# Kernel tuning notes

Measured on AMD Instinct MI355X. Metric: run time of the kernel, lower is better.

## Reference

```python
import jax, jax.numpy as jnp
import numpy as np

B, C_IN, T = 64, 9, 4096
HIDDEN, OUT = 128, 10
NEW_T = T // 4            # two MaxPool1d(2) stages
N_NODES = B * NEW_T       # 65536 flattened nodes
N_EDGES = 524288


def setup_inputs() -> dict:
    key = jax.random.key(0)
    ks = jax.random.split(key, 8)
    def w(k, sh, fan):
        return jax.random.normal(k, sh, jnp.float32) * (1.0 / np.sqrt(fan))
    return {
        "x": jax.random.normal(ks[0], (B, C_IN, T), jnp.float32),
        "edge_index": jax.random.randint(ks[1], (2, N_EDGES), 0, N_NODES, dtype=jnp.int32),
        "conv1_w": w(ks[2], (16, C_IN, 5), C_IN * 5),
        "conv1_b": jnp.zeros((16,), jnp.float32),
        "conv2_w": w(ks[3], (32, 16, 5), 16 * 5),
        "conv2_b": jnp.zeros((32,), jnp.float32),
        "gcn1_w": w(ks[4], (32, HIDDEN), 32),
        "gcn1_b": jnp.zeros((HIDDEN,), jnp.float32),
        "gcn2_w": w(ks[5], (HIDDEN, HIDDEN), HIDDEN),
        "gcn2_b": jnp.zeros((HIDDEN,), jnp.float32),
        "cls_w": w(ks[6], (HIDDEN, OUT), HIDDEN),
        "cls_b": jnp.zeros((OUT,), jnp.float32),
    }


def _conv1d(x, w, b):
    # x: [B, C, T], w: [O, I, K], 'same' padding (pad=2, k=5)
    y = jax.lax.conv_general_dilated(x, w, (1,), [(2, 2)],
                                     dimension_numbers=("NCH", "OIH", "NCH"))
    return y + b[None, :, None]


def _maxpool2(x):
    return jax.lax.reduce_window(x, -jnp.inf, jax.lax.max, (1, 1, 2), (1, 1, 2), "VALID")


def _gcn(x, w, b, src, dst):
    # PyG GCNConv: add self-loops, symmetric D^{-1/2}(A+I)D^{-1/2} X W + b
    h = x @ w
    deg = jnp.zeros((N_NODES,), x.dtype).at[dst].add(1.0) + 1.0  # +1 for self-loop
    dinv = jax.lax.rsqrt(deg)
    coef = dinv[src] * dinv[dst]                      # [E]
    agg = jnp.zeros_like(h).at[dst].add(h[src] * coef[:, None])
    agg = agg + h * (dinv * dinv)[:, None]            # self-loop contribution
    return agg + b


def reference(x, edge_index, conv1_w, conv1_b, conv2_w, conv2_b,
              gcn1_w, gcn1_b, gcn2_w, gcn2_b, cls_w, cls_b):
    h = _maxpool2(jax.nn.relu(_conv1d(x, conv1_w, conv1_b)))   # [B,16,T/2]
    h = _maxpool2(jax.nn.relu(_conv1d(h, conv2_w, conv2_b)))   # [B,32,T/4]
    feats = h.transpose(0, 2, 1).reshape(-1, 32)               # [B*NEW_T, 32]
    src, dst = edge_index[0], edge_index[1]
    g = jax.nn.relu(_gcn(feats, gcn1_w, gcn1_b, src, dst))
    g = jax.nn.relu(_gcn(g, gcn2_w, gcn2_b, src, dst))
    pooled = g.reshape(B, NEW_T, HIDDEN).mean(axis=1)          # mean over nodes per graph
    return pooled @ cls_w + cls_b                              # [B, OUT]
```

## Files before the change

### kernel.cpp

```cpp
#include <hip/hip_runtime.h>
#include <hip/hip_bf16.h>

typedef __hip_bfloat16 bf16;
typedef unsigned short ushort8_v __attribute__((ext_vector_type(8)));
typedef short bf16x8 __attribute__((ext_vector_type(8)));
typedef float f32x4 __attribute__((ext_vector_type(4)));

#define N_B     64
#define C_IN    9
#define T0      4096
#define C1      16
#define T1      2048
#define C2      32
#define T2      1024
#define N_NODES 65536
#define N_EDGES 524288
#define HID     128
#define OUT_C   10
#define SLOT_CAP 32

__device__ __forceinline__ float us2f(unsigned short u) {
  union { unsigned int i; float f; } c; c.i = ((unsigned int)u) << 16; return c.f;
}
__device__ __forceinline__ unsigned short f2us(float f) {
  bf16 h = __float2bfloat16(f);
  unsigned short u;
  __builtin_memcpy(&u, &h, 2);
  return u;
}


__global__ __launch_bounds__(256) void init_kernel(int* __restrict__ cnt, float* __restrict__ pooled,
                                                   const float* __restrict__ W1, const float* __restrict__ W2,
                                                   unsigned short* __restrict__ W1T, unsigned short* __restrict__ W2T)
{
  int gid = blockIdx.x * 256 + threadIdx.x;
  if (gid < N_NODES) cnt[gid] = 0;
  if (gid < N_B * HID) pooled[gid] = 0.f;
  if (gid < HID * HID) {
    int j = gid >> 7, k = gid & 127;
    W2T[j * HID + k] = f2us(W2[(size_t)k * HID + j]);
  }
  if (gid >= 32768 && gid < 32768 + HID * 32) {
    int i = gid - 32768;
    int j = i >> 5, k = i & 31;
    W1T[j * 32 + k] = f2us(W1[(size_t)k * HID + j]);
  }
}

__global__ __launch_bounds__(256) void conv1_scatter_kernel(const float* __restrict__ x, const float* __restrict__ w1,
                                                            const float* __restrict__ b1,
                                                            const int* __restrict__ ei, int* __restrict__ cnt,
                                                            unsigned short* __restrict__ slots,
                                                            unsigned short* __restrict__ y1)
{
  __shared__ float sx[C_IN * 136];
  __shared__ float sw[45 * 17];
  __shared__ float sb[C1];
  int tid = threadIdx.x;
  if (blockIdx.x < 2048) {
    int e = blockIdx.x * 256 + tid;
    int d = ei[N_EDGES + e];
    int s = ei[e];
    int r = atomicAdd(&cnt[d], 1);
    if (r < SLOT_CAP) slots[((size_t)d << 5) + r] = (unsigned short)s;
    return;
  }
  int blk = blockIdx.x - 2048;
  int b = blk >> 5;
  int P0 = (blk & 31) << 6;
  int t0 = 2 * P0 - 2;
  for (int i = tid; i < C_IN * 132; i += 256) {
    int c = i / 132, j = i % 132;
    int t = t0 + j;
    sx[c * 136 + j] = (t >= 0 && t < T0) ? x[(size_t)(b * C_IN + c) * T0 + t] : 0.f;
  }
  for (int i = tid; i < C1 * 45; i += 256) sw[(i % 45) * 17 + i / 45] = w1[i];
  if (tid < C1) sb[tid] = b1[tid];
  __syncthreads();

  int o = tid & 15, pg = tid >> 4;
  float bias = sb[o];
  float a[8];
  #pragma unroll
  for (int i = 0; i < 8; ++i) a[i] = bias;
  #pragma unroll
  for (int c = 0; c < C_IN; ++c) {
    float xv[12];
    #pragma unroll
    for (int q = 0; q < 3; ++q)
      *(float4*)&xv[4 * q] = *(const float4*)&sx[c * 136 + 8 * pg + 4 * q];
    const float* wr = &sw[(c * 5) * 17 + o];
    float w0 = wr[0], w1_ = wr[17], w2_ = wr[34], w3_ = wr[51], w4_ = wr[68];
    #pragma unroll
    for (int m = 0; m < 8; ++m)
      a[m] += xv[m]*w0 + xv[m+1]*w1_ + xv[m+2]*w2_ + xv[m+3]*w3_ + xv[m+4]*w4_;
  }
  ushort4 r;
  r.x = f2us(fmaxf(fmaxf(a[0], a[1]), 0.f));
  r.y = f2us(fmaxf(fmaxf(a[2], a[3]), 0.f));
  r.z = f2us(fmaxf(fmaxf(a[4], a[5]), 0.f));
  r.w = f2us(fmaxf(fmaxf(a[6], a[7]), 0.f));
  *(ushort4*)&y1[(size_t)(b * C1 + o) * T1 + P0 + 4 * pg] = r;
}

__global__ __launch_bounds__(256) void conv2_kernel(const unsigned short* __restrict__ y1, const float* __restrict__ w2,
                                                    const float* __restrict__ b2, const int* __restrict__ cnt,
                                                    unsigned short* __restrict__ feats)
{
  __shared__ float sy[C1 * 72];
  __shared__ float sw[80 * 33];
  __shared__ float sb[C2];
  int tid = threadIdx.x;
  int b = blockIdx.x >> 5;
  int Q0 = (blockIdx.x & 31) << 5;
  int t0 = 2 * Q0 - 2;
  for (int i = tid; i < C1 * 68; i += 256) {
    int c = i / 68, j = i % 68;
    int t = t0 + j;
    sy[c * 72 + j] = (t >= 0 && t < T1) ? us2f(y1[(size_t)(b * C1 + c) * T1 + t]) : 0.f;
  }
  for (int i = tid; i < C2 * 80; i += 256) sw[(i % 80) * 33 + i / 80] = w2[i];
  if (tid < C2) sb[tid] = b2[tid];
  __syncthreads();

  int o = tid & 31, pg = tid >> 5;
  float bias = sb[o];
  float a[8];
  #pragma unroll
  for (int i = 0; i < 8; ++i) a[i] = bias;
  #pragma unroll
  for (int c = 0; c < C1; ++c) {
    float yv[12];
    #pragma unroll
    for (int q = 0; q < 3; ++q)
      *(float4*)&yv[4 * q] = *(const float4*)&sy[c * 72 + 8 * pg + 4 * q];
    const float* wr = &sw[(c * 5) * 33 + o];
    float w0 = wr[0], w1_ = wr[33], w2_ = wr[66], w3_ = wr[99], w4_ = wr[132];
    #pragma unroll
    for (int m = 0; m < 8; ++m)
      a[m] += yv[m]*w0 + yv[m+1]*w1_ + yv[m+2]*w2_ + yv[m+3]*w3_ + yv[m+4]*w4_;
  }
  #pragma unroll
  for (int i = 0; i < 4; ++i) {
    int node = (b << 10) + Q0 + 4 * pg + i;
    float dv = rsqrtf((float)cnt[node] + 1.0f);
    feats[(size_t)node * C2 + o] = f2us(fmaxf(fmaxf(a[2*i], a[2*i+1]), 0.f) * dv);
  }
}

__global__ __launch_bounds__(256) void aggX_kernel(const unsigned short* __restrict__ F, const int* __restrict__ cnt,
                                                   const unsigned short* __restrict__ slots,
                                                   unsigned short* __restrict__ aggXb)
{
  int tid = threadIdx.x;
  int node = (blockIdx.x << 6) + (tid >> 2);
  int jq = (tid & 3) << 3;
  int cn = cnt[node];
  float dn = rsqrtf((float)cn + 1.0f);
  float acc[8];
  {
    ushort8_v r = *(const ushort8_v*)(F + (size_t)node * C2 + jq);
    #pragma unroll
    for (int k = 0; k < 8; ++k) acc[k] = us2f(r[k]);
  }
  const unsigned short* sl = slots + ((size_t)node << 5);
  int e1 = min(cn, SLOT_CAP);
  int e = 0;
  for (; e + 2 <= e1; e += 2) {
    int s0 = sl[e], s1 = sl[e + 1];
    ushort8_v r0 = *(const ushort8_v*)(F + (size_t)s0 * C2 + jq);
    ushort8_v r1 = *(const ushort8_v*)(F + (size_t)s1 * C2 + jq);
    #pragma unroll
    for (int k = 0; k < 8; ++k) acc[k] += us2f(r0[k]) + us2f(r1[k]);
  }
  if (e < e1) {
    int s0 = sl[e];
    ushort8_v r0 = *(const ushort8_v*)(F + (size_t)s0 * C2 + jq);
    #pragma unroll
    for (int k = 0; k < 8; ++k) acc[k] += us2f(r0[k]);
  }
  ushort8_v o;
  #pragma unroll
  for (int k = 0; k < 8; ++k) o[k] = f2us(acc[k] * dn);
  *(ushort8_v*)(aggXb + (size_t)node * C2 + jq) = o;
}

__global__ __launch_bounds__(256) void gemm12_kernel(const unsigned short* __restrict__ aggXb,
                                                     const unsigned short* __restrict__ W1T,
                                                     const float* __restrict__ gb1,
                                                     const unsigned short* __restrict__ W2T,
                                                     const int* __restrict__ cnt,
                                                     unsigned short* __restrict__ Hb)
{
  __shared__ unsigned short sG[64 * 132];
  int tid = threadIdx.x;
  int w = tid >> 6, l = tid & 63;
  int lr = l & 15, lk = l >> 4;
  int n0b = blockIdx.x << 6;

  {
    int nb = w << 4;
    bf16x8 af = *(const bf16x8*)((const short*)aggXb + (size_t)(n0b + nb + lr) * C2 + lk * 8);
    #pragma unroll
    for (int jt = 0; jt < 8; ++jt) {
      bf16x8 bfr = *(const bf16x8*)((const short*)W1T + (jt * 16 + lr) * 32 + lk * 8);
      f32x4 acc = {0.f, 0.f, 0.f, 0.f};
      acc = __builtin_amdgcn_mfma_f32_16x16x32_bf16(af, bfr, acc, 0, 0, 0);
      float bj = gb1[jt * 16 + lr];
      #pragma unroll
      for (int r = 0; r < 4; ++r)
        sG[(nb + lk * 4 + r) * 132 + jt * 16 + lr] = f2us(fmaxf(acc[r] + bj, 0.f));
    }
  }
  __syncthreads();

  {
    int jb = w << 5;
    bf16x8 bfr[2][4];
    #pragma unroll
    for (int jtt = 0; jtt < 2; ++jtt)
      #pragma unroll
      for (int ks = 0; ks < 4; ++ks)
        bfr[jtt][ks] = *(const bf16x8*)((const short*)W2T + (size_t)(jb + jtt * 16 + lr) * HID + ks * 32 + lk * 8);
    #pragma unroll
    for (int nt = 0; nt < 4; ++nt) {
      bf16x8 afr[4];
      #pragma unroll
      for (int ks = 0; ks < 4; ++ks)
        afr[ks] = *(const bf16x8*)((const short*)sG + (nt * 16 + lr) * 132 + ks * 32 + lk * 8);
      int rowb = n0b + nt * 16 + lk * 4;
      int4 c4 = *(const int4*)&cnt[rowb];
      float dvr[4] = { rsqrtf((float)c4.x + 1.f), rsqrtf((float)c4.y + 1.f),
                       rsqrtf((float)c4.z + 1.f), rsqrtf((float)c4.w + 1.f) };
      #pragma unroll
      for (int jtt = 0; jtt < 2; ++jtt) {
        f32x4 acc = {0.f, 0.f, 0.f, 0.f};
        #pragma unroll
        for (int ks = 0; ks < 4; ++ks)
          acc = __builtin_amdgcn_mfma_f32_16x16x32_bf16(afr[ks], bfr[jtt][ks], acc, 0, 0, 0);
        #pragma unroll
        for (int r = 0; r < 4; ++r)
          Hb[(size_t)(rowb + r) * HID + jb + jtt * 16 + lr] = f2us(acc[r] * dvr[r]);
      }
    }
  }
}

__global__ __launch_bounds__(256) void agg2_pool_kernel(const unsigned short* __restrict__ Hb, const int* __restrict__ cnt,
                                                        const unsigned short* __restrict__ slots,
                                                        const float* __restrict__ bias, float* __restrict__ pooled)
{
  __shared__ float red[16][HID];
  int tid = threadIdx.x;
  int g = tid >> 4;
  int jq = (tid & 15) << 3;
  int node = (blockIdx.x << 4) + g;
  int cn = cnt[node];
  float dn = rsqrtf((float)cn + 1.0f);
  float acc[8];
  {
    ushort8_v r = *(const ushort8_v*)(Hb + (size_t)node * HID + jq);
    #pragma unroll
    for (int k = 0; k < 8; ++k) acc[k] = us2f(r[k]);
  }
  const unsigned short* sl = slots + ((size_t)node << 5);
  int e1 = min(cn, SLOT_CAP);
  int e = 0;
  for (; e + 2 <= e1; e += 2) {
    int s0 = sl[e], s1 = sl[e + 1];
    ushort8_v r0 = *(const ushort8_v*)(Hb + (size_t)s0 * HID + jq);
    ushort8_v r1 = *(const ushort8_v*)(Hb + (size_t)s1 * HID + jq);
    #pragma unroll
    for (int k = 0; k < 8; ++k) acc[k] += us2f(r0[k]) + us2f(r1[k]);
  }
  if (e < e1) {
    int s0 = sl[e];
    ushort8_v r0 = *(const ushort8_v*)(Hb + (size_t)s0 * HID + jq);
    #pragma unroll
    for (int k = 0; k < 8; ++k) acc[k] += us2f(r0[k]);
  }
  #pragma unroll
  for (int k = 0; k < 8; ++k)
    red[g][jq + k] = fmaxf(dn * acc[k] + bias[jq + k], 0.f);
  __syncthreads();
  if (tid < HID) {
    float s = 0.f;
    #pragma unroll
    for (int g2 = 0; g2 < 16; ++g2) s += red[g2][tid];
    int b = blockIdx.x >> 6;
    atomicAdd(&pooled[b * HID + tid], s * (1.0f / 1024.0f));
  }
}


__global__ __launch_bounds__(64) void cls_kernel(const float* __restrict__ pooled, const float* __restrict__ w,
                                                 const float* __restrict__ cb, float* __restrict__ out)
{
  int b = blockIdx.x, o = threadIdx.x;
  if (o < OUT_C) {
    float acc = cb[o];
    for (int i = 0; i < HID; ++i)
      acc += pooled[b * HID + i] * w[i * OUT_C + o];
    out[b * OUT_C + o] = acc;
  }
}


extern "C" void kernel_launch(void* const* d_in, const int* in_sizes, int n_in,
                              void* d_out, int out_size, void* d_ws, size_t ws_size,
                              hipStream_t stream)
{
  const float* x    = (const float*)d_in[0];
  const int*   ei   = (const int*)d_in[1];
  const float* c1w  = (const float*)d_in[2];
  const float* c1b  = (const float*)d_in[3];
  const float* c2w  = (const float*)d_in[4];
  const float* c2b  = (const float*)d_in[5];
  const float* g1w  = (const float*)d_in[6];
  const float* g1b  = (const float*)d_in[7];
  const float* g2w  = (const float*)d_in[8];
  const float* g2b  = (const float*)d_in[9];
  const float* clsw = (const float*)d_in[10];
  const float* clsb = (const float*)d_in[11];
  float* outp = (float*)d_out;

  char* ws = (char*)d_ws;
  size_t off_b = 0;
  auto alloc = [&](size_t bytes) { void* p = ws + off_b; off_b = (off_b + bytes + 255) & ~(size_t)255; return p; };
  int*   cnt    = (int*)  alloc((size_t)N_NODES * 4);
  unsigned short* slots = (unsigned short*)alloc((size_t)N_NODES * SLOT_CAP * 2);
  unsigned short* w1t   = (unsigned short*)alloc((size_t)HID * 32 * 2);
  unsigned short* w2t   = (unsigned short*)alloc((size_t)HID * HID * 2);
  unsigned short* y1    = (unsigned short*)alloc((size_t)N_B * C1 * T1 * 2);
  unsigned short* feats = (unsigned short*)alloc((size_t)N_NODES * C2 * 2);
  unsigned short* aggXb = (unsigned short*)alloc((size_t)N_NODES * C2 * 2);
  unsigned short* H     = (unsigned short*)alloc((size_t)N_NODES * HID * 2);
  float* pooled = (float*)alloc((size_t)N_B * HID * 4);
  (void)ws_size; (void)in_sizes; (void)n_in; (void)out_size;

  init_kernel         <<<256, 256, 0, stream>>>(cnt, pooled, g1w, g2w, w1t, w2t);
  conv1_scatter_kernel<<<4096, 256, 0, stream>>>(x, c1w, c1b, ei, cnt, slots, y1);

  conv2_kernel<<<2048, 256, 0, stream>>>(y1, c2w, c2b, cnt, feats);

  aggX_kernel<<<N_NODES / 64, 256, 0, stream>>>(feats, cnt, slots, aggXb);

  gemm12_kernel<<<N_NODES / 64, 256, 0, stream>>>(aggXb, w1t, g1b, w2t, cnt, H);

  agg2_pool_kernel<<<N_NODES / 16, 256, 0, stream>>>(H, cnt, slots, g2b, pooled);

  cls_kernel<<<N_B, 64, 0, stream>>>(pooled, clsw, clsb, outp);
}
```

Baseline: 110.8 us.

## Fuse first GCN aggregation into GEMM kernel and fold init work elsewhere

The separate first-layer aggregation kernel is removed. Each gemm12 lane now gathers its node's neighbor features for its 8-wide K slice and builds the MFMA A fragment directly, so the aggX intermediate never goes through global memory. The weight transposes move into extra blocks of the conv1/scatter launch, and the counter and pooled zeroing become hipMemsetAsync calls. Both gather loops are unrolled to four loads in flight. This saves a launch and an intermediate round trip, but adds two memset operations, and the gather in gemm12 may be less parallel than the old standalone kernel.

After: 107.3 us. 1.03x faster.

```diff
diff --git a/kernel.cpp b/kernel.cpp
--- a/kernel.cpp
+++ b/kernel.cpp
@@ -29,30 +29,14 @@
   return u;
 }
 
-
-__global__ __launch_bounds__(256) void init_kernel(int* __restrict__ cnt, float* __restrict__ pooled,
-                                                   const float* __restrict__ W1, const float* __restrict__ W2,
-                                                   unsigned short* __restrict__ W1T, unsigned short* __restrict__ W2T)
-{
-  int gid = blockIdx.x * 256 + threadIdx.x;
-  if (gid < N_NODES) cnt[gid] = 0;
-  if (gid < N_B * HID) pooled[gid] = 0.f;
-  if (gid < HID * HID) {
-    int j = gid >> 7, k = gid & 127;
-    W2T[j * HID + k] = f2us(W2[(size_t)k * HID + j]);
-  }
-  if (gid >= 32768 && gid < 32768 + HID * 32) {
-    int i = gid - 32768;
-    int j = i >> 5, k = i & 31;
-    W1T[j * 32 + k] = f2us(W1[(size_t)k * HID + j]);
-  }
-}
-
 __global__ __launch_bounds__(256) void conv1_scatter_kernel(const float* __restrict__ x, const float* __restrict__ w1,
                                                             const float* __restrict__ b1,
                                                             const int* __restrict__ ei, int* __restrict__ cnt,
                                                             unsigned short* __restrict__ slots,
-                                                            unsigned short* __restrict__ y1)
+                                                            unsigned short* __restrict__ y1,
+                                                            const float* __restrict__ W1, const float* __restrict__ W2,
+                                                            unsigned short* __restrict__ W1T,
+                                                            unsigned short* __restrict__ W2T)
 {
   __shared__ float sx[C_IN * 136];
   __shared__ float sw[45 * 17];
@@ -66,6 +50,26 @@
     if (r < SLOT_CAP) slots[((size_t)d << 5) + r] = (unsigned short)s;
     return;
   }
+  if (blockIdx.x >= 4096) {
+    int blk = blockIdx.x - 4096;
+    if (blk < 16) {
+      int base = blk * 1024 + tid * 4;
+      #pragma unroll
+      for (int i = 0; i < 4; ++i) {
+        int idx = base + i;
+        int j = idx >> 7, k = idx & 127;
+        W2T[j * HID + k] = f2us(W2[(size_t)k * HID + j]);
+      }
+    } else {
+      #pragma unroll
+      for (int i = 0; i < 16; ++i) {
+        int idx = tid * 16 + i;
+        int j = idx >> 5, k = idx & 31;
+        W1T[j * 32 + k] = f2us(W1[(size_t)k * HID + j]);
+      }
+    }
+    return;
+  }
   int blk = blockIdx.x - 2048;
   int b = blk >> 5;
   int P0 = (blk & 31) << 6;
@@ -149,48 +153,12 @@
   }
 }
 
-__global__ __launch_bounds__(256) void aggX_kernel(const unsigned short* __restrict__ F, const int* __restrict__ cnt,
-                                                   const unsigned short* __restrict__ slots,
-                                                   unsigned short* __restrict__ aggXb)
-{
-  int tid = threadIdx.x;
-  int node = (blockIdx.x << 6) + (tid >> 2);
-  int jq = (tid & 3) << 3;
-  int cn = cnt[node];
-  float dn = rsqrtf((float)cn + 1.0f);
-  float acc[8];
-  {
-    ushort8_v r = *(const ushort8_v*)(F + (size_t)node * C2 + jq);
-    #pragma unroll
-    for (int k = 0; k < 8; ++k) acc[k] = us2f(r[k]);
-  }
-  const unsigned short* sl = slots + ((size_t)node << 5);
-  int e1 = min(cn, SLOT_CAP);
-  int e = 0;
-  for (; e + 2 <= e1; e += 2) {
-    int s0 = sl[e], s1 = sl[e + 1];
-    ushort8_v r0 = *(const ushort8_v*)(F + (size_t)s0 * C2 + jq);
-    ushort8_v r1 = *(const ushort8_v*)(F + (size_t)s1 * C2 + jq);
-    #pragma unroll
-    for (int k = 0; k < 8; ++k) acc[k] += us2f(r0[k]) + us2f(r1[k]);
-  }
-  if (e < e1) {
-    int s0 = sl[e];
-    ushort8_v r0 = *(const ushort8_v*)(F + (size_t)s0 * C2 + jq);
-    #pragma unroll
-    for (int k = 0; k < 8; ++k) acc[k] += us2f(r0[k]);
-  }
-  ushort8_v o;
-  #pragma unroll
-  for (int k = 0; k < 8; ++k) o[k] = f2us(acc[k] * dn);
-  *(ushort8_v*)(aggXb + (size_t)node * C2 + jq) = o;
-}
-
-__global__ __launch_bounds__(256) void gemm12_kernel(const unsigned short* __restrict__ aggXb,
+__global__ __launch_bounds__(256) void gemm12_kernel(const unsigned short* __restrict__ F,
+                                                     const int* __restrict__ cnt,
+                                                     const unsigned short* __restrict__ slots,
                                                      const unsigned short* __restrict__ W1T,
                                                      const float* __restrict__ gb1,
                                                      const unsigned short* __restrict__ W2T,
-                                                     const int* __restrict__ cnt,
                                                      unsigned short* __restrict__ Hb)
 {
   __shared__ unsigned short sG[64 * 132];
@@ -201,7 +169,39 @@
 
   {
     int nb = w << 4;
-    bf16x8 af = *(const bf16x8*)((const short*)aggXb + (size_t)(n0b + nb + lr) * C2 + lk * 8);
+    int node = n0b + nb + lr;
+    int cn = cnt[node];
+    float dn = rsqrtf((float)cn + 1.0f);
+    int koff = lk << 3;
+    float accf[8];
+    {
+      ushort8_v r = *(const ushort8_v*)(F + (size_t)node * C2 + koff);
+      #pragma unroll
+      for (int k = 0; k < 8; ++k) accf[k] = us2f(r[k]);
+    }
+    const unsigned short* sl = slots + ((size_t)node << 5);
+    int e1 = min(cn, SLOT_CAP);
+    int e = 0;
+    for (; e + 4 <= e1; e += 4) {
+      int s0 = sl[e], s1 = sl[e + 1], s2 = sl[e + 2], s3 = sl[e + 3];
+      ushort8_v r0 = *(const ushort8_v*)(F + (size_t)s0 * C2 + koff);
+      ushort8_v r1 = *(const ushort8_v*)(F + (size_t)s1 * C2 + koff);
+      ushort8_v r2 = *(const ushort8_v*)(F + (size_t)s2 * C2 + koff);
+      ushort8_v r3 = *(const ushort8_v*)(F + (size_t)s3 * C2 + koff);
+      #pragma unroll
+      for (int k = 0; k < 8; ++k)
+        accf[k] += (us2f(r0[k]) + us2f(r1[k])) + (us2f(r2[k]) + us2f(r3[k]));
+    }
+    for (; e < e1; ++e) {
+      int s0 = sl[e];
+      ushort8_v r0 = *(const ushort8_v*)(F + (size_t)s0 * C2 + koff);
+      #pragma unroll
+      for (int k = 0; k < 8; ++k) accf[k] += us2f(r0[k]);
+    }
+    bf16x8 af;
+    #pragma unroll
+    for (int k = 0; k < 8; ++k) af[k] = (short)f2us(accf[k] * dn);
+
     #pragma unroll
     for (int jt = 0; jt < 8; ++jt) {
       bf16x8 bfr = *(const bf16x8*)((const short*)W1T + (jt * 16 + lr) * 32 + lk * 8);
@@ -267,14 +267,17 @@
   const unsigned short* sl = slots + ((size_t)node << 5);
   int e1 = min(cn, SLOT_CAP);
   int e = 0;
-  for (; e + 2 <= e1; e += 2) {
-    int s0 = sl[e], s1 = sl[e + 1];
+  for (; e + 4 <= e1; e += 4) {
+    int s0 = sl[e], s1 = sl[e + 1], s2 = sl[e + 2], s3 = sl[e + 3];
     ushort8_v r0 = *(const ushort8_v*)(Hb + (size_t)s0 * HID + jq);
     ushort8_v r1 = *(const ushort8_v*)(Hb + (size_t)s1 * HID + jq);
-    #pragma unroll
-    for (int k = 0; k < 8; ++k) acc[k] += us2f(r0[k]) + us2f(r1[k]);
-  }
-  if (e < e1) {
+    ushort8_v r2 = *(const ushort8_v*)(Hb + (size_t)s2 * HID + jq);
+    ushort8_v r3 = *(const ushort8_v*)(Hb + (size_t)s3 * HID + jq);
+    #pragma unroll
+    for (int k = 0; k < 8; ++k)
+      acc[k] += (us2f(r0[k]) + us2f(r1[k])) + (us2f(r2[k]) + us2f(r3[k]));
+  }
+  for (; e < e1; ++e) {
     int s0 = sl[e];
     ushort8_v r0 = *(const ushort8_v*)(Hb + (size_t)s0 * HID + jq);
     #pragma unroll
@@ -334,19 +337,18 @@
   unsigned short* w2t   = (unsigned short*)alloc((size_t)HID * HID * 2);
   unsigned short* y1    = (unsigned short*)alloc((size_t)N_B * C1 * T1 * 2);
   unsigned short* feats = (unsigned short*)alloc((size_t)N_NODES * C2 * 2);
-  unsigned short* aggXb = (unsigned short*)alloc((size_t)N_NODES * C2 * 2);
   unsigned short* H     = (unsigned short*)alloc((size_t)N_NODES * HID * 2);
   float* pooled = (float*)alloc((size_t)N_B * HID * 4);
   (void)ws_size; (void)in_sizes; (void)n_in; (void)out_size;
 
-  init_kernel         <<<256, 256, 0, stream>>>(cnt, pooled, g1w, g2w, w1t, w2t);
-  conv1_scatter_kernel<<<4096, 256, 0, stream>>>(x, c1w, c1b, ei, cnt, slots, y1);
+  hipMemsetAsync(cnt, 0, (size_t)N_NODES * 4, stream);
+  hipMemsetAsync(pooled, 0, (size_t)N_B * HID * 4, stream);
+
+  conv1_scatter_kernel<<<4113, 256, 0, stream>>>(x, c1w, c1b, ei, cnt, slots, y1, g1w, g2w, w1t, w2t);
 
   conv2_kernel<<<2048, 256, 0, stream>>>(y1, c2w, c2b, cnt, feats);
 
-  aggX_kernel<<<N_NODES / 64, 256, 0, stream>>>(feats, cnt, slots, aggXb);
-
-  gemm12_kernel<<<N_NODES / 64, 256, 0, stream>>>(aggXb, w1t, g1b, w2t, cnt, H);
+  gemm12_kernel<<<N_NODES / 64, 256, 0, stream>>>(feats, cnt, slots, w1t, g1b, w2t, H);
 
   agg2_pool_kernel<<<N_NODES / 16, 256, 0, stream>>>(H, cnt, slots, g2b, pooled);
 
```
